# Kernel optimization log

Measured on AMD Instinct MI355X. Metric: run time of the kernel, lower is better.

Reference implementation:

```python
import jax, jax.numpy as jnp
import numpy as np

HEADS = 8
HIDDEN = 512
SEQ = 1024
BATCH = 8
SCALE = 1.2
TOPK = round(0.05 * SEQ)  # 51, as in mode='stocastic'


def setup_inputs() -> dict:
    key = jax.random.key(0)
    ks = jax.random.split(key, 12)
    d = HIDDEN
    s = 0.02
    return {
        "Query_x": jax.random.normal(ks[0], (BATCH, SEQ, d), jnp.float32),
        "KeyandValue_x": jax.random.normal(ks[1], (BATCH, SEQ, d), jnp.float32),
        "Wq": jax.random.normal(ks[2], (d, d), jnp.float32) * s,
        "bq": jnp.zeros((d,), jnp.float32),
        "Wk": jax.random.normal(ks[3], (d, d), jnp.float32) * s,
        "bk": jnp.zeros((d,), jnp.float32),
        "Wv": jax.random.normal(ks[4], (d, d), jnp.float32) * s,
        "bv": jnp.zeros((d,), jnp.float32),
        "Wo": jax.random.normal(ks[5], (d, d), jnp.float32) * s,
        "bo": jnp.zeros((d,), jnp.float32),
        "randidx": jax.random.randint(ks[6], (round(0.1 * SEQ),), 0, SEQ, jnp.int32),
    }


def _split_heads(x, B, S):
    # torch: split last dim into heads chunks, cat along dim 0 -> [heads*B, S, dk]
    dk = HIDDEN // HEADS
    return x.reshape(B, S, HEADS, dk).transpose(2, 0, 1, 3).reshape(HEADS * B, S, dk)


def _merge_heads(x, B, S):
    dk = HIDDEN // HEADS
    return x.reshape(HEADS, B, S, dk).transpose(1, 2, 0, 3).reshape(B, S, HIDDEN)


def moderate_attention(a, randidx):
    # a: [N, S, L] softmaxed attention. Scale top-k + random columns by SCALE,
    # then renormalize rows. torch scatter_ writes a*SCALE gathered from the
    # pre-scatter tensor, so duplicate indices are idempotent -> boolean mask.
    N, S, L = a.shape
    _, idx = jax.lax.top_k(a, TOPK)                       # [N, S, k]
    rand_b = jnp.broadcast_to(randidx.astype(idx.dtype), (N, S, randidx.shape[0]))
    all_idx = jnp.concatenate([idx, rand_b], axis=-1)      # [N, S, k+r]
    n_ix = jnp.arange(N)[:, None, None]
    q_ix = jnp.arange(S)[None, :, None]
    sel = jnp.zeros(a.shape, bool).at[n_ix, q_ix, all_idx].set(True)
    a2 = jnp.where(sel, a * SCALE, a)
    return a2 / jnp.sum(a2, axis=-1, keepdims=True)


def reference(Query_x, KeyandValue_x, Wq, bq, Wk, bk, Wv, bv, Wo, bo, randidx):
    B, S, _ = Query_x.shape
    dk = HIDDEN // HEADS
    Q = _split_heads(Query_x @ Wq + bq, B, S)          # [H*B, S, dk]
    K = _split_heads(KeyandValue_x @ Wk + bk, B, S)
    V = _split_heads(KeyandValue_x @ Wv + bv, B, S)
    scores = jnp.einsum('nqd,nkd->nqk', Q, K) / jnp.sqrt(jnp.float32(dk))
    a = jax.nn.softmax(scores, axis=-1)
    a = moderate_attention(a, randidx)
    out = jnp.einsum('nqk,nkd->nqd', a, V)
    return _merge_heads(out, B, S) @ Wo + bo
```

## Files before the change

### kernel.cpp

```cpp
#include <hip/hip_runtime.h>
#include <stdint.h>

typedef unsigned short ushort_t;
typedef __bf16 bf16x8 __attribute__((ext_vector_type(8)));
typedef _Float16 f16x8v __attribute__((ext_vector_type(8)));
typedef __fp16 fp16x2 __attribute__((ext_vector_type(2)));
typedef float f32x4 __attribute__((ext_vector_type(4)));

#define SEQ   1024
#define DK    64
#define TOPK_N 51
#define RSCALE 1.2f
#define LOG2E    1.44269504089f
#define LOG2_12  0.26303440583f

#define OFF_WT  0
#define OFF_Q   (4*512*512)
#define OFF_K   (OFF_Q  + 64*1024*64)
#define OFF_V   (OFF_K  + 64*1024*64)
#define OFF_A   (OFF_V  + 64*1024*64)
#define OFF_MASK (OFF_A + 8192*512)

static __device__ __forceinline__ ushort_t f2bf(float f){
  union { float f; unsigned u; } x; x.f = f;
  unsigned r = x.u + 0x7FFFu + ((x.u >> 16) & 1u);
  return (ushort_t)(r >> 16);
}
static __device__ __forceinline__ ushort_t f2h(float f){
  union { _Float16 h; ushort_t u; } x; x.h = (_Float16)f; return x.u;
}
static __device__ __forceinline__ float h2f(ushort_t u){
  union { ushort_t u; _Float16 h; } x; x.u = u; return (float)x.h;
}
static __device__ __forceinline__ unsigned pk2(float a, float b){
  union { fp16x2 h; unsigned u; } x;
  x.h = __builtin_amdgcn_cvt_pkrtz(a, b);
  return x.u;
}
static __device__ __forceinline__ unsigned pkrne(float a, float b){
  return (unsigned)f2h(a) | ((unsigned)f2h(b) << 16);
}
static __device__ __forceinline__ bf16x8 frag16(const ushort_t* p){
  union { uint4 u; bf16x8 b; } x; x.u = *(const uint4*)p; return x.b;
}
static __device__ __forceinline__ f16x8v frag16h(const ushort_t* p){
  union { uint4 u; f16x8v h; } x; x.u = *(const uint4*)p; return x.h;
}
static __device__ __forceinline__ void gll16(const ushort_t* g, ushort_t* lds){
  __builtin_amdgcn_global_load_lds((const __attribute__((address_space(1))) unsigned*)g,
                                   (__attribute__((address_space(3))) unsigned*)lds,
                                   16, 0, 0);
}

__global__ __launch_bounds__(256) void prep_k(
    const float* Wq, const float* Wk, const float* Wv, const float* Wo,
    const int* ridx, int nrand, ushort_t* ws){
  __shared__ ushort_t t[64][72];
  __shared__ unsigned wds[64];
  int bid = blockIdx.x, tid = threadIdx.x;

  if (bid < 256){
    int rb = bid;
    int z = rb >> 6, rem = rb & 63;
    const float* W = z==0?Wq: z==1?Wk: z==2?Wv: Wo;
    ushort_t* O = ws + OFF_WT + (size_t)z*512*512;
    int kt = (rem >> 3)*64, nt = (rem & 7)*64;
    int r0 = tid>>3, c8 = (tid&7)*8;
    #pragma unroll
    for (int p=0;p<2;p++){
      int r = p*32 + r0;
      float4 a = *(const float4*)&W[(size_t)(kt+r)*512 + nt + c8];
      float4 b = *(const float4*)&W[(size_t)(kt+r)*512 + nt + c8 + 4];
      t[r][c8+0]=f2bf(a.x); t[r][c8+1]=f2bf(a.y); t[r][c8+2]=f2bf(a.z); t[r][c8+3]=f2bf(a.w);
      t[r][c8+4]=f2bf(b.x); t[r][c8+5]=f2bf(b.y); t[r][c8+6]=f2bf(b.z); t[r][c8+7]=f2bf(b.w);
    }
    __syncthreads();
    #pragma unroll
    for (int p=0;p<2;p++){
      int r = p*32 + r0;
      union { ushort_t s[8]; uint4 u; } tmp;
      #pragma unroll
      for (int j=0;j<8;j++) tmp.s[j] = t[c8+j][r];
      *(uint4*)&O[(size_t)(nt+r)*512 + kt + c8] = tmp.u;
    }
  } else {
    if (tid < 64) wds[tid] = 0;
    __syncthreads();
    for (int i = tid; i < nrand; i += 256){
      int col = ridx[i];
      atomicOr(&wds[(col >> 3) & 63], 1u << (((col >> 9) << 3) | (col & 7)));
    }
    __syncthreads();
    if (tid < 64) (ws + OFF_MASK)[tid] = (ushort_t)wds[tid];
  }
}

__global__ __launch_bounds__(256, 2) void gemmqkv_k(ushort_t* ws,
    const float* qx, const float* kvx,
    const float* bq, const float* bk, const float* bv){
  bool isKV = (blockIdx.z != 0);
  const float* Xf = isKV ? kvx : qx;
  const ushort_t* WT0 = ws + OFF_WT + (size_t)(isKV ? 1 : 0)*512*512;
  const ushort_t* WT1 = ws + OFF_WT + (size_t)2*512*512;

  __shared__ ushort_t sA [2][128*32];
  __shared__ ushort_t sB0[3][128*32];
  __shared__ ushort_t sB1[3][128*32];
  int tid = threadIdx.x, lane = tid & 63, w = tid >> 6;
  int wm = w & 1, wn = w >> 1;
  int m0 = blockIdx.y * 128, n0 = blockIdx.x * 128;
  int r16 = lane & 15, quad = lane >> 4;
  int srow = tid >> 2, sch = tid & 3;
  int arow = tid >> 1, acp = (tid & 1) * 2;

  const f32x4 zero = {0.f,0.f,0.f,0.f};
  f32x4 acc0[4][4], acc1[4][4];
  #pragma unroll
  for (int i=0;i<4;i++)
    #pragma unroll
    for (int j=0;j<4;j++){ acc0[i][j] = zero; acc1[i][j] = zero; }

  #define STAGE_B(WT, t, buf, SB)                                              \
    {                                                                          \
      int k0 = (t)*32;                                                         \
      _Pragma("unroll")                                                        \
      for (int p=0;p<2;p++){                                                   \
        int row = p*64 + srow;                                                 \
        int gch = sch ^ ((row >> 1) & 3);                                      \
        gll16(WT + (size_t)(n0+row)*512 + k0 + gch*8, &SB[buf][(p*64 + (w<<4))*32]); \
      }                                                                        \
    }
  #define AISSUE(t, rg)                                                        \
    {                                                                          \
      int k0 = (t)*32;                                                         \
      _Pragma("unroll")                                                        \
      for (int c=0;c<2;c++){                                                   \
        int lc = (acp + c) ^ ((arow >> 1) & 3);                                \
        const float* sp = Xf + (size_t)(m0+arow)*512 + k0 + lc*8;              \
        rg[c*2+0] = *(const float4*)sp;                                        \
        rg[c*2+1] = *(const float4*)(sp + 4);                                  \
      }                                                                        \
    }
  #define AWRITE(buf, rg)                                                      \
    {                                                                          \
      _Pragma("unroll")                                                        \
      for (int c=0;c<2;c++){                                                   \
        union { ushort_t s[8]; uint4 u; } pkk;                                 \
        pkk.s[0]=f2bf(rg[c*2+0].x); pkk.s[1]=f2bf(rg[c*2+0].y);                \
        pkk.s[2]=f2bf(rg[c*2+0].z); pkk.s[3]=f2bf(rg[c*2+0].w);                \
        pkk.s[4]=f2bf(rg[c*2+1].x); pkk.s[5]=f2bf(rg[c*2+1].y);                \
        pkk.s[6]=f2bf(rg[c*2+1].z); pkk.s[7]=f2bf(rg[c*2+1].w);                \
        *(uint4*)&sA[buf][arow*32 + (acp + c)*8] = pkk.u;                      \
      }                                                                        \
    }

  float4 rg[4];
  AISSUE(0, rg);
  STAGE_B(WT0, 0, 0, sB0);
  if (isKV) STAGE_B(WT1, 0, 0, sB1);

  for (int t = 0; t < 16; t++){
    float4 rn[4];
    if (t < 15){
      AISSUE(t+1, rn);
      STAGE_B(WT0, t+1, (t+1)%3, sB0);
      if (isKV){
        STAGE_B(WT1, t+1, (t+1)%3, sB1);
        asm volatile("s_waitcnt vmcnt(8)" ::: "memory");
      } else {
        asm volatile("s_waitcnt vmcnt(6)" ::: "memory");
      }
    } else {
      asm volatile("s_waitcnt vmcnt(0)" ::: "memory");
    }
    int abuf = t & 1, bbuf = t % 3;
    AWRITE(abuf, rg);
    asm volatile("s_waitcnt lgkmcnt(0)" ::: "memory");
    __builtin_amdgcn_s_barrier();
    asm volatile("" ::: "memory");
    bf16x8 aF[4], bF[4];
    #pragma unroll
    for (int i=0;i<4;i++){
      int row = wm*64 + i*16 + r16;
      aF[i] = frag16(&sA[abuf][row*32 + ((quad ^ ((row >> 1) & 3))*8)]);
    }
    #pragma unroll
    for (int j=0;j<4;j++){
      int row = wn*64 + j*16 + r16;
      bF[j] = frag16(&sB0[bbuf][row*32 + ((quad ^ ((row >> 1) & 3))*8)]);
    }
    __builtin_amdgcn_s_setprio(1);
    #pragma unroll
    for (int i=0;i<4;i++)
      #pragma unroll
      for (int j=0;j<4;j++)
        acc0[i][j] = __builtin_amdgcn_mfma_f32_16x16x32_bf16(aF[i], bF[j], acc0[i][j], 0,0,0);
    __builtin_amdgcn_s_setprio(0);
    if (isKV){
      #pragma unroll
      for (int j=0;j<4;j++){
        int row = wn*64 + j*16 + r16;
        bF[j] = frag16(&sB1[bbuf][row*32 + ((quad ^ ((row >> 1) & 3))*8)]);
      }
      __builtin_amdgcn_s_setprio(1);
      #pragma unroll
      for (int i=0;i<4;i++)
        #pragma unroll
        for (int j=0;j<4;j++)
          acc1[i][j] = __builtin_amdgcn_mfma_f32_16x16x32_bf16(aF[i], bF[j], acc1[i][j], 0,0,0);
      __builtin_amdgcn_s_setprio(0);
    }
    #pragma unroll
    for (int c=0;c<4;c++) rg[c] = rn[c];
  }
  #undef STAGE_B
  #undef AISSUE
  #undef AWRITE

  #pragma unroll
  for (int i=0;i<4;i++){
    int rowbase = m0 + wm*64 + i*16 + quad*4;
    #pragma unroll
    for (int j=0;j<4;j++){
      int col = n0 + wn*64 + j*16 + r16;
      int h = col >> 6, d = col & 63;
      if (!isKV){
        float bsv = bq[col];
        ushort_t* out = ws + OFF_Q;
        #pragma unroll
        for (int r=0;r<4;r++){
          int row = rowbase + r;
          int b = row >> 10, s = row & 1023;
          int nh = h*8 + b;
          out[ ((size_t)nh*1024 + s)*64 + d ] = f2bf((acc0[i][j][r] + bsv)*0.125f);
        }
      } else {
        {
          float bsv = bk[col];
          ushort_t* out = ws + OFF_K;
          int b = rowbase >> 10;
          int nh = h*8 + b;
          size_t base = (size_t)nh*65536 + (size_t)(d>>3)*8192 + (d&7);
          #pragma unroll
          for (int r=0;r<4;r++){
            int s = (rowbase + r) & 1023;
            out[ base + (size_t)s*8 ] = f2bf(acc0[i][j][r] + bsv);
          }
        }
        {
          float bsv = bv[col];
          ushort_t* out = ws + OFF_V;
          int b = rowbase >> 10, s = rowbase & 1023;
          int nh = h*8 + b;
          union { ushort_t sh[4]; uint2 u2; } pk;
          #pragma unroll
          for (int r=0;r<4;r++) pk.sh[r] = f2h(acc1[i][j][r] + bsv);
          *(uint2*)&out[ (((size_t)nh*128 + (s>>3))*64 + d)*8 + (s&4) ] = pk.u2;
        }
      }
    }
  }
}

__global__ __launch_bounds__(256, 3) void gemm3_k(ushort_t* ws,
    const float* bo, float* dout){
  const ushort_t* Xb = ws + OFF_A;
  const ushort_t* WT = ws + OFF_WT + (size_t)3*(512*512);

  __shared__ ushort_t sA[3][128*32];
  __shared__ ushort_t sB[3][128*32];
  int tid = threadIdx.x, lane = tid & 63, w = tid >> 6;
  int wm = w & 1, wn = w >> 1;
  int m0 = blockIdx.y * 128, n0 = blockIdx.x * 128;
  int r16 = lane & 15, quad = lane >> 4;
  int srow = tid >> 2, sch = tid & 3;

  const f32x4 zero = {0.f,0.f,0.f,0.f};
  f32x4 acc[4][4];
  #pragma unroll
  for (int i=0;i<4;i++)
    #pragma unroll
    for (int j=0;j<4;j++) acc[i][j] = zero;

  #define STAGE(t, buf)                                                        \
    {                                                                          \
      int k0 = (t)*32;                                                         \
      _Pragma("unroll")                                                        \
      for (int p=0;p<2;p++){                                                   \
        int row = p*64 + srow;                                                 \
        int gch = sch ^ ((row >> 1) & 3);                                      \
        gll16(Xb + (size_t)(m0+row)*512 + k0 + gch*8, &sA[buf][(p*64 + (w<<4))*32]); \
        gll16(WT + (size_t)(n0+row)*512 + k0 + gch*8, &sB[buf][(p*64 + (w<<4))*32]); \
      }                                                                        \
    }

  STAGE(0, 0);
  STAGE(1, 1);
  #pragma unroll
  for (int t = 0; t < 16; t++){
    if (t < 15) asm volatile("s_waitcnt vmcnt(4)" ::: "memory");
    else        asm volatile("s_waitcnt vmcnt(0)" ::: "memory");
    __builtin_amdgcn_s_barrier();
    asm volatile("" ::: "memory");
    if (t < 14) STAGE(t+2, (t+2)%3);
    int buf = t % 3;
    bf16x8 aF[4], bF[4];
    #pragma unroll
    for (int i=0;i<4;i++){
      int row = wm*64 + i*16 + r16;
      aF[i] = frag16(&sA[buf][row*32 + ((quad ^ ((row >> 1) & 3))*8)]);
    }
    #pragma unroll
    for (int j=0;j<4;j++){
      int row = wn*64 + j*16 + r16;
      bF[j] = frag16(&sB[buf][row*32 + ((quad ^ ((row >> 1) & 3))*8)]);
    }
    __builtin_amdgcn_s_setprio(1);
    #pragma unroll
    for (int i=0;i<4;i++)
      #pragma unroll
      for (int j=0;j<4;j++)
        acc[i][j] = __builtin_amdgcn_mfma_f32_16x16x32_bf16(aF[i], bF[j], acc[i][j], 0,0,0);
    __builtin_amdgcn_s_setprio(0);
  }
  #undef STAGE

  #pragma unroll
  for (int i=0;i<4;i++){
    int rowbase = m0 + wm*64 + i*16 + quad*4;
    #pragma unroll
    for (int j=0;j<4;j++){
      int col = n0 + wn*64 + j*16 + r16;
      float bsv = bo[col];
      #pragma unroll
      for (int r=0;r<4;r++)
        dout[(size_t)(rowbase+r)*512 + col] = acc[i][j][r] + bsv;
    }
  }
}

__global__ __launch_bounds__(256, 4) void attn_k(const ushort_t* ws_q, const ushort_t* ws_k,
     const ushort_t* ws_v, const ushort_t* maskp, ushort_t* attn){
  __shared__ __align__(16) ushort_t sS[16*1024];

  int tid = threadIdx.x, lane = tid&63, w = tid>>6;
  int r16 = lane&15, quad = lane>>4;
  int gid = blockIdx.x;
  int n  = (gid & 7)*8 + ((gid >> 3) >> 6);
  int q0 = ((gid >> 3) & 63) * 16;
  const ushort_t* Qn = ws_q + (size_t)n*SEQ*DK;
  const ushort_t* Kn = ws_k + (size_t)n*SEQ*DK;
  const ushort_t* Vb = ws_v + (size_t)n*SEQ*DK;

  unsigned rmask = (unsigned)maskp[lane];

  bf16x8 aQ[2];
  #pragma unroll
  for (int t=0;t<2;t++)
    aQ[t] = frag16(Qn + (size_t)(q0 + r16)*64 + t*32 + quad*8);

  const f32x4 zero = {0.f,0.f,0.f,0.f};

  #pragma unroll
  for (int half=0; half<2; half++){
    f32x4 acc[8];
    #pragma unroll
    for (int i=0;i<8;i++) acc[i] = zero;
    #pragma unroll
    for (int grp=0; grp<2; grp++){
      int c = half*2 + grp;
      bf16x8 bF[8];
      #pragma unroll
      for (int u=0;u<4;u++){
        int key = c*256 + w*64 + u*16 + r16;
        bF[u*2+0] = frag16(Kn + ((size_t)(quad    )*1024 + key)*8);
        bF[u*2+1] = frag16(Kn + ((size_t)(4 + quad)*1024 + key)*8);
      }
      __builtin_amdgcn_s_setprio(1);
      #pragma unroll
      for (int u=0;u<4;u++){
        int t8 = grp*4 + u;
        acc[t8] = __builtin_amdgcn_mfma_f32_16x16x32_bf16(bF[u*2+0], aQ[0], acc[t8], 0,0,0);
        acc[t8] = __builtin_amdgcn_mfma_f32_16x16x32_bf16(bF[u*2+1], aQ[1], acc[t8], 0,0,0);
      }
      __builtin_amdgcn_s_setprio(0);
    }
    int rs = r16 & 7;
    #pragma unroll
    for (int grp=0; grp<2; grp++)
      #pragma unroll
      for (int u=0;u<4;u++){
        int kb = (half*2+grp)*256 + w*64 + u*16 + quad*4;
        f32x4 a = acc[grp*4+u];
        uint2 o;
        o.x = pkrne(a[0], a[1]);
        o.y = pkrne(a[2], a[3]);
        *(uint2*)(sS + r16*1024 + (((kb>>3) ^ rs) << 3) + (kb & 4)) = o;
      }
  }
  __syncthreads();

  float v[4][16];
  float vmax[4];
  #pragma unroll
  for (int r=0;r<4;r++){
    int row = w*4 + r, rs = row & 7;
    const ushort_t* bp = sS + row*1024 + ((lane ^ rs) * 8);
    uint4 lo4 = *(const uint4*)bp;
    uint4 hi4 = *(const uint4*)(bp + 512);
    unsigned wl[8] = {lo4.x, lo4.y, lo4.z, lo4.w, hi4.x, hi4.y, hi4.z, hi4.w};
    float m = -3.0e38f;
    #pragma unroll
    for (int k=0;k<8;k++){
      float a = h2f((ushort_t)(wl[k] & 0xffffu));
      float b = h2f((ushort_t)(wl[k] >> 16));
      v[r][2*k] = a; v[r][2*k+1] = b;
      m = fmaxf(m, fmaxf(a, b));
    }
    vmax[r] = m;
  }
  #pragma unroll
  for (int r=0;r<4;r++)
    #pragma unroll
    for (int j=0;j<16;j++)
      asm volatile("" : "+v"(v[r][j]));

  #pragma unroll
  for (int off=32; off>=1; off>>=1)
    #pragma unroll
    for (int r=0;r<4;r++) vmax[r] = fmaxf(vmax[r], __shfl_xor(vmax[r], off));

  float blo[4], bhi[4];
  #pragma unroll
  for (int r=0;r<4;r++){ bhi[r] = vmax[r]; blo[r] = vmax[r] - 1.0f; }
  #pragma unroll 1
  for (int it=0; it<9; it++){
    #pragma unroll
    for (int r=0;r<4;r++){
      float mid = 0.5f*(blo[r]+bhi[r]);
      int cnt = 0;
      #pragma unroll
      for (int j=0;j<16;j++)
        cnt += __popcll(__ballot(v[r][j] >= mid));
      bool ge = (cnt >= TOPK_N);
      blo[r] = ge ? mid : blo[r];
      bhi[r] = ge ? bhi[r] : mid;
    }
  }
  float fb[16];
  #pragma unroll
  for (int j=0;j<16;j++) fb[j] = ((rmask >> j) & 1u) ? LOG2_12 : 0.0f;
  float sC = LOG2_12;
  asm volatile("" : "+v"(sC));

  float ls[4];
  #pragma unroll
  for (int r=0;r<4;r++){
    float thr = blo[r], s = 0.f;
    #pragma unroll
    for (int j=0;j<16;j++){
      float tb = (v[r][j] >= thr) ? sC : fb[j];
      float e = __builtin_amdgcn_exp2f(
                  __builtin_fmaf(v[r][j] - vmax[r], LOG2E, tb));
      v[r][j] = e; s += e;
    }
    ls[r] = s;
  }
  #pragma unroll
  for (int off=32; off>=1; off>>=1)
    #pragma unroll
    for (int r=0;r<4;r++) ls[r] += __shfl_xor(ls[r], off);
  #pragma unroll
  for (int r=0;r<4;r++){
    int row = w*4 + r, rs = row & 7;
    float rinv = 1.0f / ls[r];
    ushort_t* bp = sS + row*1024 + ((lane ^ rs) * 8);
    uint4 o0, o1;
    o0.x = pk2(v[r][0]*rinv,  v[r][1]*rinv);
    o0.y = pk2(v[r][2]*rinv,  v[r][3]*rinv);
    o0.z = pk2(v[r][4]*rinv,  v[r][5]*rinv);
    o0.w = pk2(v[r][6]*rinv,  v[r][7]*rinv);
    o1.x = pk2(v[r][8]*rinv,  v[r][9]*rinv);
    o1.y = pk2(v[r][10]*rinv, v[r][11]*rinv);
    o1.z = pk2(v[r][12]*rinv, v[r][13]*rinv);
    o1.w = pk2(v[r][14]*rinv, v[r][15]*rinv);
    *(uint4*)bp = o0;
    *(uint4*)(bp + 512) = o1;
  }
  __syncthreads();

  f32x4 oa0 = zero, oa1 = zero;
  int dd = w*16 + r16;
  #pragma unroll
  for (int kb2=0; kb2<8; kb2++){
    f16x8v bV[4], aP[4];
    #pragma unroll
    for (int u=0;u<4;u++){
      int g8 = (kb2*4 + u)*4 + quad;
      bV[u] = frag16h(Vb + ((size_t)g8*64 + dd)*8);
      aP[u] = frag16h(sS + r16*1024 + ((g8 ^ (r16&7))*8));
    }
    __builtin_amdgcn_s_setprio(1);
    #pragma unroll
    for (int u=0;u<4;u++){
      if (u&1) oa1 = __builtin_amdgcn_mfma_f32_16x16x32_f16(aP[u], bV[u], oa1, 0,0,0);
      else     oa0 = __builtin_amdgcn_mfma_f32_16x16x32_f16(aP[u], bV[u], oa0, 0,0,0);
    }
    __builtin_amdgcn_s_setprio(0);
  }
  f32x4 oacc = oa0 + oa1;

  int h = n >> 3, b = n & 7;
  #pragma unroll
  for (int r=0;r<4;r++){
    int s = q0 + quad*4 + r;
    attn[ ((size_t)(b*1024 + s))*512 + h*64 + w*16 + r16 ] = f2bf(oacc[r]);
  }
}

extern "C" void kernel_launch(void* const* d_in, const int* in_sizes, int n_in,
                              void* d_out, int out_size, void* d_ws, size_t ws_size,
                              hipStream_t stream){
  const float* Qx  = (const float*)d_in[0];
  const float* KVx = (const float*)d_in[1];
  const float* Wq  = (const float*)d_in[2];
  const float* bq  = (const float*)d_in[3];
  const float* Wk  = (const float*)d_in[4];
  const float* bk  = (const float*)d_in[5];
  const float* Wv  = (const float*)d_in[6];
  const float* bv  = (const float*)d_in[7];
  const float* Wo  = (const float*)d_in[8];
  const float* bo  = (const float*)d_in[9];
  const int* ridx  = (const int*)d_in[10];
  int nrand = in_sizes[10];
  ushort_t* ws = (ushort_t*)d_ws;
  float* dout = (float*)d_out;

  prep_k<<<257, 256, 0, stream>>>(Wq, Wk, Wv, Wo, ridx, nrand, ws);
  gemmqkv_k<<<dim3(4,64,2), 256, 0, stream>>>(ws, Qx, KVx, bq, bk, bv);
  attn_k<<<4096, 256, 0, stream>>>(ws+OFF_Q, ws+OFF_K, ws+OFF_V, ws+OFF_MASK, ws+OFF_A);
  gemm3_k<<<dim3(4,64,1), 256, 0, stream>>>(ws, bo, dout);
}
```

Before: 215.1 us.

## Prefetch A tiles two steps ahead and swizzle block mapping in GEMMs

The QKV projection GEMM now keeps two register sets for the fp32 A tile and issues the global load for step t+2 right after writing step t to shared memory. This gives the loads more time in flight than the old one-step prefetch. Both the QKV and output-projection GEMMs also remap the linear block id so that consecutively scheduled blocks share column tiles in a grouped order, aiming for better L2 reuse of weights and activations. The deeper prefetch raises register pressure and relies on the hand-tuned vmcnt counts staying correct.

Result: no change. 216.6 us (+0.7%).

```diff
diff --git a/kernel.cpp b/kernel.cpp
--- a/kernel.cpp
+++ b/kernel.cpp
@@ -108,7 +108,9 @@
   __shared__ ushort_t sB1[3][128*32];
   int tid = threadIdx.x, lane = tid & 63, w = tid >> 6;
   int wm = w & 1, wn = w >> 1;
-  int m0 = blockIdx.y * 128, n0 = blockIdx.x * 128;
+  int id = blockIdx.x + (blockIdx.y << 2);
+  int m0 = (((id & 7) << 3) + (id >> 5)) * 128;
+  int n0 = ((id >> 3) & 3) * 128;
   int r16 = lane & 15, quad = lane >> 4;
   int srow = tid >> 2, sch = tid & 3;
   int arow = tid >> 1, acp = (tid & 1) * 2;
@@ -154,65 +156,72 @@
       }                                                                        \
     }
 
-  float4 rg[4];
-  AISSUE(0, rg);
+  #define QKV_STEP(t_, rg)                                                     \
+  {                                                                            \
+    if ((t_) < 15){                                                            \
+      STAGE_B(WT0, (t_)+1, ((t_)+1)%3, sB0);                                   \
+      if (isKV){                                                               \
+        STAGE_B(WT1, (t_)+1, ((t_)+1)%3, sB1);                                 \
+        asm volatile("s_waitcnt vmcnt(8)" ::: "memory");                       \
+      } else {                                                                 \
+        asm volatile("s_waitcnt vmcnt(6)" ::: "memory");                       \
+      }                                                                        \
+    } else {                                                                   \
+      asm volatile("s_waitcnt vmcnt(0)" ::: "memory");                         \
+    }                                                                          \
+    AWRITE((t_) & 1, rg);                                                      \
+    if ((t_) < 14) AISSUE((t_)+2, rg);             \
+    asm volatile("s_waitcnt lgkmcnt(0)" ::: "memory");                         \
+    __builtin_amdgcn_s_barrier();                                              \
+    asm volatile("" ::: "memory");                                             \
+    {                                                                          \
+      int abuf = (t_) & 1, bbuf = (t_) % 3;                                    \
+      bf16x8 aF[4], bF[4];                                                     \
+      _Pragma("unroll")                                                        \
+      for (int i=0;i<4;i++){                                                   \
+        int row = wm*64 + i*16 + r16;                                          \
+        aF[i] = frag16(&sA[abuf][row*32 + ((quad ^ ((row >> 1) & 3))*8)]);     \
+      }                                                                        \
+      _Pragma("unroll")                                                        \
+      for (int j=0;j<4;j++){                                                   \
+        int row = wn*64 + j*16 + r16;                                          \
+        bF[j] = frag16(&sB0[bbuf][row*32 + ((quad ^ ((row >> 1) & 3))*8)]);    \
+      }                                                                        \
+      __builtin_amdgcn_s_setprio(1);                                           \
+      _Pragma("unroll")                                                        \
+      for (int i=0;i<4;i++)                                                    \
+        _Pragma("unroll")                                                      \
+        for (int j=0;j<4;j++)                                                  \
+          acc0[i][j] = __builtin_amdgcn_mfma_f32_16x16x32_bf16(aF[i], bF[j], acc0[i][j], 0,0,0); \
+      __builtin_amdgcn_s_setprio(0);                                           \
+      if (isKV){                                                               \
+        _Pragma("unroll")                                                      \
+        for (int j=0;j<4;j++){                                                 \
+          int row = wn*64 + j*16 + r16;                                        \
+          bF[j] = frag16(&sB1[bbuf][row*32 + ((quad ^ ((row >> 1) & 3))*8)]);  \
+        }                                                                      \
+        __builtin_amdgcn_s_setprio(1);                                         \
+        _Pragma("unroll")                                                      \
+        for (int i=0;i<4;i++)                                                  \
+          _Pragma("unroll")                                                    \
+          for (int j=0;j<4;j++)                                                \
+            acc1[i][j] = __builtin_amdgcn_mfma_f32_16x16x32_bf16(aF[i], bF[j], acc1[i][j], 0,0,0); \
+        __builtin_amdgcn_s_setprio(0);                                         \
+      }                                                                        \
+    }                                                                          \
+  }
+
+  float4 rgA[4], rgB[4];
+  AISSUE(0, rgA);
   STAGE_B(WT0, 0, 0, sB0);
   if (isKV) STAGE_B(WT1, 0, 0, sB1);
-
-  for (int t = 0; t < 16; t++){
-    float4 rn[4];
-    if (t < 15){
-      AISSUE(t+1, rn);
-      STAGE_B(WT0, t+1, (t+1)%3, sB0);
-      if (isKV){
-        STAGE_B(WT1, t+1, (t+1)%3, sB1);
-        asm volatile("s_waitcnt vmcnt(8)" ::: "memory");
-      } else {
-        asm volatile("s_waitcnt vmcnt(6)" ::: "memory");
-      }
-    } else {
-      asm volatile("s_waitcnt vmcnt(0)" ::: "memory");
-    }
-    int abuf = t & 1, bbuf = t % 3;
-    AWRITE(abuf, rg);
-    asm volatile("s_waitcnt lgkmcnt(0)" ::: "memory");
-    __builtin_amdgcn_s_barrier();
-    asm volatile("" ::: "memory");
-    bf16x8 aF[4], bF[4];
-    #pragma unroll
-    for (int i=0;i<4;i++){
-      int row = wm*64 + i*16 + r16;
-      aF[i] = frag16(&sA[abuf][row*32 + ((quad ^ ((row >> 1) & 3))*8)]);
-    }
-    #pragma unroll
-    for (int j=0;j<4;j++){
-      int row = wn*64 + j*16 + r16;
-      bF[j] = frag16(&sB0[bbuf][row*32 + ((quad ^ ((row >> 1) & 3))*8)]);
-    }
-    __builtin_amdgcn_s_setprio(1);
-    #pragma unroll
-    for (int i=0;i<4;i++)
-      #pragma unroll
-      for (int j=0;j<4;j++)
-        acc0[i][j] = __builtin_amdgcn_mfma_f32_16x16x32_bf16(aF[i], bF[j], acc0[i][j], 0,0,0);
-    __builtin_amdgcn_s_setprio(0);
-    if (isKV){
-      #pragma unroll
-      for (int j=0;j<4;j++){
-        int row = wn*64 + j*16 + r16;
-        bF[j] = frag16(&sB1[bbuf][row*32 + ((quad ^ ((row >> 1) & 3))*8)]);
-      }
-      __builtin_amdgcn_s_setprio(1);
-      #pragma unroll
-      for (int i=0;i<4;i++)
-        #pragma unroll
-        for (int j=0;j<4;j++)
-          acc1[i][j] = __builtin_amdgcn_mfma_f32_16x16x32_bf16(aF[i], bF[j], acc1[i][j], 0,0,0);
-      __builtin_amdgcn_s_setprio(0);
-    }
-    #pragma unroll
-    for (int c=0;c<4;c++) rg[c] = rn[c];
-  }
+  AISSUE(1, rgB);
+
+  for (int tt = 0; tt < 8; tt++){
+    QKV_STEP(tt*2,     rgA);
+    QKV_STEP(tt*2 + 1, rgB);
+  }
+  #undef QKV_STEP
   #undef STAGE_B
   #undef AISSUE
   #undef AWRITE
@@ -271,7 +280,9 @@
   __shared__ ushort_t sB[3][128*32];
   int tid = threadIdx.x, lane = tid & 63, w = tid >> 6;
   int wm = w & 1, wn = w >> 1;
-  int m0 = blockIdx.y * 128, n0 = blockIdx.x * 128;
+  int id = blockIdx.x + (blockIdx.y << 2);
+  int m0 = (((id & 7) << 3) + (id >> 5)) * 128;
+  int n0 = ((id >> 3) & 3) * 128;
   int r16 = lane & 15, quad = lane >> 4;
   int srow = tid >> 2, sch = tid & 3;
 
```
